# Kernel optimization log

Measured on AMD Instinct MI355X. Metric: run time of the kernel, lower is better.

Reference implementation:

```python
import jax, jax.numpy as jnp
import numpy as np

B, L, C = 8, 4096, 512
WS, SHIFT, H = 64, 32, 16
HD = C // H
HID = 4 * C


def _ln(x, w, b):
    m = x.mean(-1, keepdims=True)
    v = ((x - m) ** 2).mean(-1, keepdims=True)
    return (x - m) / jnp.sqrt(v + 1e-5) * w + b


def _attn_mask():
    # 0 / -100 mask for shifted windows, shape (nW, WS, WS)
    img = np.zeros((L,), np.float32)
    cnt = 0
    for s in (slice(0, L - WS), slice(L - WS, L - SHIFT), slice(L - SHIFT, L)):
        img[s] = cnt
        cnt += 1
    mw = img.reshape(L // WS, WS)
    d = mw[:, :, None] - mw[:, None, :]
    return jnp.asarray(np.where(d != 0, -100.0, 0.0).astype(np.float32))


def _cpb_coords():
    # log-spaced continuous relative coords, shape (2*WS-1, 1)
    r = np.arange(-(WS - 1), WS, dtype=np.float32) / (WS - 1) * 8.0
    t = np.sign(r) * np.log2(np.abs(r) + 1.0) / np.log2(8.0)
    return jnp.asarray(t[:, None].astype(np.float32))


def _rel_index():
    c = np.arange(WS)
    return jnp.asarray((c[:, None] - c[None, :] + WS - 1).astype(np.int32))


def setup_inputs():
    key = jax.random.key(0)
    ks = jax.random.split(key, 8)
    n = jax.random.normal
    return {
        "x": n(ks[0], (B, L, C), jnp.float32),
        "qkv_w": n(ks[1], (3 * C, C), jnp.float32) * 0.02,
        "q_bias": jnp.zeros((C,), jnp.float32),
        "v_bias": jnp.zeros((C,), jnp.float32),
        "logit_scale": jnp.log(10.0 * jnp.ones((H, 1, 1), jnp.float32)),
        "cpb_w1": n(ks[2], (512, 1), jnp.float32) * 0.02,
        "cpb_b1": jnp.zeros((512,), jnp.float32),
        "cpb_w2": n(ks[3], (H, 512), jnp.float32) * 0.02,
        "proj_w": n(ks[4], (C, C), jnp.float32) * 0.02,
        "proj_b": jnp.zeros((C,), jnp.float32),
        "norm1_w": jnp.ones((C,), jnp.float32),
        "norm1_b": jnp.zeros((C,), jnp.float32),
        "norm2_w": jnp.ones((C,), jnp.float32),
        "norm2_b": jnp.zeros((C,), jnp.float32),
        "fc1_w": n(ks[5], (HID, C), jnp.float32) * 0.02,
        "fc1_b": jnp.zeros((HID,), jnp.float32),
        "fc2_w": n(ks[6], (C, HID), jnp.float32) * 0.02,
        "fc2_b": jnp.zeros((C,), jnp.float32),
    }


def reference(x, qkv_w, q_bias, v_bias, logit_scale, cpb_w1, cpb_b1, cpb_w2,
              proj_w, proj_b, norm1_w, norm1_b, norm2_w, norm2_b,
              fc1_w, fc1_b, fc2_w, fc2_b):
    nW = L // WS
    shortcut = x
    # cyclic shift + window partition
    xs = jnp.roll(x, -SHIFT, axis=1)
    xw = xs.reshape(B * nW, WS, C)
    # qkv with q/v bias only (k bias is zero)
    qkv_b = jnp.concatenate([q_bias, jnp.zeros_like(v_bias), v_bias])
    qkv = (xw @ qkv_w.T + qkv_b).reshape(B * nW, WS, 3, H, HD)
    qkv = qkv.transpose(2, 0, 3, 1, 4)  # (3, B*nW, H, WS, HD)
    q, k, v = qkv[0], qkv[1], qkv[2]
    # cosine attention with learned, clamped per-head temperature
    qn = q / jnp.maximum(jnp.linalg.norm(q, axis=-1, keepdims=True), 1e-12)
    kn = k / jnp.maximum(jnp.linalg.norm(k, axis=-1, keepdims=True), 1e-12)
    attn = jnp.einsum('whnd,whmd->whnm', qn, kn)
    scale = jnp.exp(jnp.minimum(logit_scale, jnp.log(100.0)))  # (H,1,1)
    attn = attn * scale
    # continuous relative position bias via small MLP
    tbl = jax.nn.relu(_cpb_coords() @ cpb_w1.T + cpb_b1) @ cpb_w2.T  # (2WS-1, H)
    bias = tbl[_rel_index()]  # (WS, WS, H)
    bias = 16.0 * jax.nn.sigmoid(bias.transpose(2, 0, 1))  # (H, WS, WS)
    attn = attn + bias[None]
    # shift mask (0 / -100), per window
    mask = _attn_mask()  # (nW, WS, WS)
    attn = attn.reshape(B, nW, H, WS, WS) + mask[None, :, None]
    attn = jax.nn.softmax(attn.reshape(B * nW, H, WS, WS), axis=-1)
    out = jnp.einsum('whnm,whmd->whnd', attn, v)
    out = out.transpose(0, 2, 1, 3).reshape(B * nW, WS, C)
    out = out @ proj_w.T + proj_b
    # window reverse + reverse shift
    out = jnp.roll(out.reshape(B, L, C), SHIFT, axis=1)
    # Swin v2 post-norm residuals
    x1 = shortcut + _ln(out, norm1_w, norm1_b)
    h = jax.nn.gelu(x1 @ fc1_w.T + fc1_b, approximate=False) @ fc2_w.T + fc2_b
    return x1 + _ln(h, norm2_w, norm2_b)
```

## Files before the change

kernel.cpp:

```cpp
#include <hip/hip_runtime.h>
#include <hip/hip_bf16.h>
#include <math.h>

typedef unsigned short u16;
typedef __bf16 bf16x8 __attribute__((ext_vector_type(8)));
typedef float f32x4 __attribute__((ext_vector_type(4)));
typedef unsigned short u16x8 __attribute__((ext_vector_type(8)));
typedef unsigned short u16x4 __attribute__((ext_vector_type(4)));
typedef unsigned short u16x2 __attribute__((ext_vector_type(2)));

#define DEV static __device__ __forceinline__

DEV float b2f(u16 v) { unsigned u = ((unsigned)v) << 16; return __builtin_bit_cast(float, u); }
DEV u16 f2bf(float f) {
  unsigned u = __builtin_bit_cast(unsigned, f);
  u += 0x7fffu + ((u >> 16) & 1u);
  return (u16)(u >> 16);
}

DEV void async16(const void* g, void* l) {
  __builtin_amdgcn_global_load_lds(
      (const __attribute__((address_space(1))) void*)g,
      (__attribute__((address_space(3))) void*)l, 16, 0, 0);
}

__global__ __launch_bounds__(256) void cvt_kernel(
    const float* __restrict__ in, u16* __restrict__ out, int n4)
{
  const int i = blockIdx.x * 256 + threadIdx.x;
  if (i < n4) {
    float4 v = ((const float4*)in)[i];
    u16x4 o;
    o[0] = f2bf(v.x); o[1] = f2bf(v.y); o[2] = f2bf(v.z); o[3] = f2bf(v.w);
    ((u16x4*)out)[i] = o;
  }
}

__global__ __launch_bounds__(64) void cpb_kernel(
    const float* __restrict__ w1, const float* __restrict__ b1,
    const float* __restrict__ w2, float* __restrict__ btbl)
{
  const int h = blockIdx.x;
  const int lane = threadIdx.x;
  __shared__ float tbl[127];
  for (int r = lane; r < 127; r += 64) {
    float rv = (float)(r - 63) * (8.0f / 63.0f);
    float sgn = (rv > 0.f) ? 1.f : ((rv < 0.f) ? -1.f : 0.f);
    float t = sgn * log2f(fabsf(rv) + 1.f) * (1.f / 3.f);
    float acc = 0.f;
    for (int k = 0; k < 512; ++k) {
      float hid = fmaxf(t * w1[k] + b1[k], 0.f);
      acc += hid * w2[h * 512 + k];
    }
    tbl[r] = acc;
  }
  __syncthreads();
  for (int idx = lane; idx < 4096; idx += 64) {
    int i = idx >> 6, j = idx & 63;
    float v = tbl[i - j + 63];
    btbl[h * 4096 + idx] = 16.f / (1.f + __expf(-v));
  }
}

template <int MODE>
__global__ __launch_bounds__(512, 2) void gemm_bt(
    const u16* __restrict__ A, const u16* __restrict__ W,
    const float* __restrict__ bias1, const float* __restrict__ bias2,
    u16* __restrict__ out, int M, int N, int K)
{
  extern __shared__ __attribute__((aligned(16))) u16 smem[];
  const int tid = threadIdx.x;
  const int lane = tid & 63;
  const int wv = tid >> 6;
  const int m0 = blockIdx.x * 256;
  const int n0 = blockIdx.y * 256;
  const int wm = (wv >> 2) * 128;
  const int wn = (wv & 3) * 64;
  const int fr = lane & 15;
  const int hi = lane >> 4;
  const int srow = tid >> 3;
  const int kb = (tid & 7) ^ (srow & 7);
  f32x4 acc[8][4] = {};

  auto stageA = [&](int buf, int k0, int i) {
    const int r = srow + (i << 6);
    const u16* src;
    if constexpr (MODE == 0) {
      const int mg = m0 + r;
      const int bb = mg >> 12;
      const int p = mg & 4095;
      const long ga = ((long)bb << 12) + ((p + 32) & 4095);
      src = A + ga * (long)K + k0 + kb * 8;
    } else if constexpr (MODE == 1) {
      const int kk = k0 + kb * 8;
      src = A + (size_t)(kk >> 5) * 1048576 + (size_t)(m0 + r) * 32 + (kk & 31);
    } else {
      src = A + (size_t)(m0 + r) * K + k0 + kb * 8;
    }
    async16(src, smem + buf * 16384 + ((i << 9) + tid) * 8);
  };
  auto stageB = [&](int buf, int k0, int i) {
    const int r = srow + (i << 6);
    async16(W + (size_t)(n0 + r) * K + k0 + kb * 8,
            smem + 32768 + buf * 16384 + ((i << 9) + tid) * 8);
  };
  auto stage_part = [&](int buf, int k0, int part) {
    if (part == 0)      { stageB(buf, k0, 0); stageB(buf, k0, 1); }
    else if (part == 1) { stageB(buf, k0, 2); stageB(buf, k0, 3); }
    else if (part == 2) { stageA(buf, k0, 0); stageA(buf, k0, 2); }
    else                { stageA(buf, k0, 1); stageA(buf, k0, 3); }
  };

  auto phase_compute = [&](const u16* lac, const u16* lbc, int mh, int ks) {
    bf16x8 fa[4], fb[4];
    const int sw = hi + (ks << 2);
    #pragma unroll
    for (int mi = 0; mi < 4; ++mi) {
      const int r = wm + ((mh << 2) + mi) * 16 + fr;
      fa[mi] = *(const bf16x8*)&lac[r * 64 + ((sw ^ (r & 7)) << 3)];
    }
    #pragma unroll
    for (int ni = 0; ni < 4; ++ni) {
      const int r = wn + ni * 16 + fr;
      fb[ni] = *(const bf16x8*)&lbc[r * 64 + ((sw ^ (r & 7)) << 3)];
    }
    asm volatile("s_waitcnt lgkmcnt(0)" ::: "memory");
    __builtin_amdgcn_sched_barrier(0);
    __builtin_amdgcn_s_setprio(1);
    #pragma unroll
    for (int mi = 0; mi < 4; ++mi)
      #pragma unroll
      for (int ni = 0; ni < 4; ++ni)
        acc[(mh << 2) + mi][ni] = __builtin_amdgcn_mfma_f32_16x16x32_bf16(
            fa[mi], fb[ni], acc[(mh << 2) + mi][ni], 0, 0, 0);
    __builtin_amdgcn_s_setprio(0);
  };

  const int NT = K >> 6;
  stage_part(0, 0, 0); stage_part(0, 0, 1); stage_part(0, 0, 2); stage_part(0, 0, 3);
  int cur = 0;
  for (int kt = 0; kt < NT; ++kt) {
    const bool hn = (kt + 1) < NT;
    const int nk0 = (kt + 1) << 6;
    const u16* lac = smem + cur * 16384;
    const u16* lbc = smem + 32768 + cur * 16384;
    const int nb = cur ^ 1;
    asm volatile("s_waitcnt vmcnt(2)" ::: "memory");
    __builtin_amdgcn_s_barrier();
    if (hn) stage_part(nb, nk0, 0);
    phase_compute(lac, lbc, 0, 0);
    if (hn) { asm volatile("s_waitcnt vmcnt(2)" ::: "memory"); }
    else    { asm volatile("s_waitcnt vmcnt(0)" ::: "memory"); }
    __builtin_amdgcn_s_barrier();
    if (hn) stage_part(nb, nk0, 1);
    phase_compute(lac, lbc, 1, 0);
    if (hn) stage_part(nb, nk0, 2);
    phase_compute(lac, lbc, 0, 1);
    if (hn) stage_part(nb, nk0, 3);
    phase_compute(lac, lbc, 1, 1);
    cur ^= 1;
  }

  const int lrow = hi * 4;
  #pragma unroll
  for (int mi = 0; mi < 8; ++mi) {
    #pragma unroll
    for (int ni = 0; ni < 4; ++ni) {
      const int n = n0 + wn + ni * 16 + fr;
      #pragma unroll
      for (int r = 0; r < 4; ++r) {
        const int m = m0 + wm + mi * 16 + lrow + r;
        float v = acc[mi][ni][r];
        if constexpr (MODE == 0) {
          const int which = n >> 9, c = n & 511;
          const int hh = c >> 5, d = c & 31;
          float bias = (which == 0) ? bias1[c] : (which == 2 ? bias2[c] : 0.f);
          const int g = m >> 6, ii = m & 63;
          out[(size_t)which * 16777216 + (size_t)g * 32768 + hh * 2048 + ii * 32 + d] =
              f2bf(v + bias);
        } else if constexpr (MODE == 2) {
          float t = v + bias1[n];
          float u = t * t;
          float z = t * (1.5957691216f + 0.0713548163f * u);
          float ge = t / (1.f + __expf(-z));
          out[(size_t)m * N + n] = f2bf(ge);
        } else {
          out[(size_t)m * N + n] = f2bf(v + bias1[n]);
        }
      }
    }
  }
}

__global__ __launch_bounds__(256) void gemm_sm3(
    const u16* __restrict__ A, const u16* __restrict__ W,
    const float* __restrict__ bias1,
    u16* __restrict__ out, int M, int N, int K)
{
  __shared__ __attribute__((aligned(16))) u16 lA[2][8192];
  __shared__ __attribute__((aligned(16))) u16 lB[2][8192];
  const int tid = threadIdx.x;
  const int wid = tid >> 6;
  const int lane = tid & 63;
  const int m0 = blockIdx.x * 128;
  const int n0 = blockIdx.y * 128;
  const int wm = (wid >> 1) * 64;
  const int wn = (wid & 1) * 64;
  f32x4 acc[4][4] = {};

  const int srow8 = lane >> 3;
  const int kel = ((lane & 7) ^ srow8) * 8;

  auto stage = [&](int b, int k0) {
    #pragma unroll
    for (int cc = 0; cc < 4; ++cc) {
      const int rb = wid * 32 + cc * 8;
      const int r = rb + srow8;
      async16(A + (size_t)(m0 + r) * K + k0 + kel, &lA[b][rb * 64]);
      async16(W + (size_t)(n0 + r) * K + k0 + kel, &lB[b][rb * 64]);
    }
  };

  const int NT = K >> 6;
  stage(0, 0);
  __syncthreads();
  int cur = 0;
  const int fr = lane & 15;
  const int hi = lane >> 4;
  const int fsw = fr & 7;
  for (int kt = 0; kt < NT; ++kt) {
    if (kt + 1 < NT) stage(cur ^ 1, (kt + 1) << 6);
    #pragma unroll
    for (int ks = 0; ks < 2; ++ks) {
      bf16x8 fa[4], fb[4];
      #pragma unroll
      for (int t = 0; t < 4; ++t) {
        const int ra = wm + t * 16 + fr;
        fa[t] = *(const bf16x8*)&lA[cur][ra * 64 + (((hi + 4 * ks) ^ fsw) << 3)];
        const int rbq = wn + t * 16 + fr;
        fb[t] = *(const bf16x8*)&lB[cur][rbq * 64 + (((hi + 4 * ks) ^ fsw) << 3)];
      }
      #pragma unroll
      for (int mi = 0; mi < 4; ++mi)
        #pragma unroll
        for (int ni = 0; ni < 4; ++ni)
          acc[mi][ni] = __builtin_amdgcn_mfma_f32_16x16x32_bf16(fa[mi], fb[ni], acc[mi][ni], 0, 0, 0);
    }
    __syncthreads();
    cur ^= 1;
  }

  const int lrow = (lane >> 4) * 4;
  #pragma unroll
  for (int mi = 0; mi < 4; ++mi)
    #pragma unroll
    for (int ni = 0; ni < 4; ++ni) {
      const int n = n0 + wn + ni * 16 + fr;
      #pragma unroll
      for (int r = 0; r < 4; ++r) {
        const int m = m0 + wm + mi * 16 + lrow + r;
        out[(size_t)m * N + n] = f2bf(acc[mi][ni][r] + bias1[n]);
      }
    }
}

__global__ __launch_bounds__(256) void attn_kernel(
    const u16* __restrict__ qkv, const float* __restrict__ ls,
    const float* __restrict__ btbl, u16* __restrict__ attnT)
{
  const int gg = blockIdx.x;
  const int w = threadIdx.x >> 6;
  const int lane = threadIdx.x & 63;
  __shared__ __attribute__((aligned(16))) u16 vt[4][2048];
  __shared__ __attribute__((aligned(16))) u16 pl[4][4096];
  const bool maskw = ((gg & 63) == 63);
  const int fr = lane & 15;
  const int fkq = (lane >> 4) * 8;
  const int crow = (lane >> 4) * 4;

  for (int t = 0; t < 4; ++t) {
    const int h = w * 4 + t;
    const size_t bgh = (size_t)gg * 32768 + (size_t)h * 2048;

    {
      const u16x8* vp = (const u16x8*)(qkv + 33554432 + bgh + (size_t)lane * 32);
      #pragma unroll
      for (int c = 0; c < 4; ++c) {
        u16x8 vr = vp[c];
        #pragma unroll
        for (int e = 0; e < 8; ++e) {
          const int d = c * 8 + e;
          const int addr = d * 64 + (((lane >> 3) ^ (d & 7)) << 3) + (lane & 7);
          vt[w][addr] = vr[e];
        }
      }
    }

    const float scale = __expf(fminf(ls[h], 4.6051701859880914f));
    bf16x8 qa[4], kb[4];
    #pragma unroll
    for (int mi = 0; mi < 4; ++mi) {
      u16x8 raw = *(const u16x8*)(qkv + bgh + (size_t)(mi * 16 + fr) * 32 + fkq);
      float f[8]; float ssum = 0.f;
      #pragma unroll
      for (int e = 0; e < 8; ++e) { f[e] = b2f(raw[e]); ssum += f[e] * f[e]; }
      ssum += __shfl_xor(ssum, 16); ssum += __shfl_xor(ssum, 32);
      const float mul = scale / fmaxf(sqrtf(ssum), 1e-12f);
      u16x8 tmp;
      #pragma unroll
      for (int e = 0; e < 8; ++e) tmp[e] = f2bf(f[e] * mul);
      qa[mi] = __builtin_bit_cast(bf16x8, tmp);
    }
    #pragma unroll
    for (int ni = 0; ni < 4; ++ni) {
      u16x8 raw = *(const u16x8*)(qkv + 16777216 + bgh + (size_t)(ni * 16 + fr) * 32 + fkq);
      float f[8]; float ssum = 0.f;
      #pragma unroll
      for (int e = 0; e < 8; ++e) { f[e] = b2f(raw[e]); ssum += f[e] * f[e]; }
      ssum += __shfl_xor(ssum, 16); ssum += __shfl_xor(ssum, 32);
      const float mul = 1.f / fmaxf(sqrtf(ssum), 1e-12f);
      u16x8 tmp;
      #pragma unroll
      for (int e = 0; e < 8; ++e) tmp[e] = f2bf(f[e] * mul);
      kb[ni] = __builtin_bit_cast(bf16x8, tmp);
    }

    f32x4 s[4][4] = {};
    __builtin_amdgcn_s_setprio(1);
    #pragma unroll
    for (int mi = 0; mi < 4; ++mi)
      #pragma unroll
      for (int ni = 0; ni < 4; ++ni)
        s[mi][ni] = __builtin_amdgcn_mfma_f32_16x16x32_bf16(qa[mi], kb[ni], s[mi][ni], 0, 0, 0);
    __builtin_amdgcn_s_setprio(0);

    const float mh = scale + 16.f;
    float inv_[4][4];
    #pragma unroll
    for (int mi = 0; mi < 4; ++mi) {
      #pragma unroll
      for (int r = 0; r < 4; ++r) {
        const int row = mi * 16 + crow + r;
        float es = 0.f;
        #pragma unroll
        for (int ni = 0; ni < 4; ++ni) {
          const int col = ni * 16 + fr;
          float sv = s[mi][ni][r] + btbl[h * 4096 + row * 64 + col];
          if (maskw && ((row < 32) != (col < 32))) sv -= 100.f;
          const float e = __expf(sv - mh);
          s[mi][ni][r] = e;
          es += e;
        }
        es += __shfl_xor(es, 1); es += __shfl_xor(es, 2);
        es += __shfl_xor(es, 4); es += __shfl_xor(es, 8);
        inv_[mi][r] = 1.f / fmaxf(es, 1e-37f);
      }
    }

    #pragma unroll
    for (int mi = 0; mi < 4; ++mi)
      #pragma unroll
      for (int r = 0; r < 4; ++r) {
        const int row = mi * 16 + crow + r;
        #pragma unroll
        for (int ni = 0; ni < 4; ++ni) {
          const int col = ni * 16 + fr;
          const int addr = row * 64 + (((col >> 3) ^ (row & 7)) << 3) + (col & 7);
          pl[w][addr] = f2bf(s[mi][ni][r]);
        }
      }
    __syncthreads();

    f32x4 o[4][2] = {};
    #pragma unroll
    for (int ks = 0; ks < 2; ++ks) {
      bf16x8 vbf[2];
      #pragma unroll
      for (int np = 0; np < 2; ++np) {
        const int d = np * 16 + fr;
        const int jb = (lane >> 4) + ks * 4;
        vbf[np] = *(const bf16x8*)&vt[w][d * 64 + ((jb ^ (d & 7)) << 3)];
      }
      __builtin_amdgcn_s_setprio(1);
      #pragma unroll
      for (int mp = 0; mp < 4; ++mp) {
        const int row = mp * 16 + fr;
        const int cb = (lane >> 4) + ks * 4;
        bf16x8 paf = *(const bf16x8*)&pl[w][row * 64 + ((cb ^ (row & 7)) << 3)];
        o[mp][0] = __builtin_amdgcn_mfma_f32_16x16x32_bf16(paf, vbf[0], o[mp][0], 0, 0, 0);
        o[mp][1] = __builtin_amdgcn_mfma_f32_16x16x32_bf16(paf, vbf[1], o[mp][1], 0, 0, 0);
      }
      __builtin_amdgcn_s_setprio(0);
    }

    #pragma unroll
    for (int mp = 0; mp < 4; ++mp)
      #pragma unroll
      for (int r = 0; r < 4; ++r) {
        const int row = mp * 16 + crow + r;
        const float iv = inv_[mp][r];
        u16* op = attnT + (size_t)h * 1048576 + (size_t)(gg * 64 + row) * 32;
        op[fr]      = f2bf(o[mp][0][r] * iv);
        op[16 + fr] = f2bf(o[mp][1][r] * iv);
      }
    __syncthreads();
  }
}

__global__ __launch_bounds__(256) void ln1_kernel(
    const u16* __restrict__ proj, const float* __restrict__ x,
    const float* __restrict__ w, const float* __restrict__ bb,
    u16* __restrict__ x1h)
{
  const int t = blockIdx.x;
  const int b = t >> 12, l = t & 4095;
  const int p = (l - 32) & 4095;
  const size_t srow = (((size_t)b << 12) + p) << 9;
  const int c0 = threadIdx.x * 2;
  u16x2 pv = *(const u16x2*)(proj + srow + c0);
  float v0 = b2f(pv[0]), v1 = b2f(pv[1]);
  float s = v0 + v1, ss = v0 * v0 + v1 * v1;
  #pragma unroll
  for (int o = 32; o > 0; o >>= 1) { s += __shfl_down(s, o); ss += __shfl_down(ss, o); }
  __shared__ float red[8];
  const int wid = threadIdx.x >> 6, lane = threadIdx.x & 63;
  if (lane == 0) { red[wid] = s; red[4 + wid] = ss; }
  __syncthreads();
  const float S = red[0] + red[1] + red[2] + red[3];
  const float SS = red[4] + red[5] + red[6] + red[7];
  const float mean = S * (1.f / 512.f);
  const float var = SS * (1.f / 512.f) - mean * mean;
  const float rstd = rsqrtf(var + 1e-5f);
  const size_t orow = (size_t)t << 9;
  float2 xv = *(const float2*)(x + orow + c0);
  const float r0 = xv.x + (v0 - mean) * rstd * w[c0] + bb[c0];
  const float r1 = xv.y + (v1 - mean) * rstd * w[c0 + 1] + bb[c0 + 1];
  u16x2 ho; ho[0] = f2bf(r0); ho[1] = f2bf(r1);
  *(u16x2*)(x1h + orow + c0) = ho;
}

__global__ __launch_bounds__(256) void ln2_kernel(
    const u16* __restrict__ fc2, const u16* __restrict__ x1h,
    const float* __restrict__ w, const float* __restrict__ bb,
    float* __restrict__ out)
{
  const int t = blockIdx.x;
  const size_t row = (size_t)t << 9;
  const int c0 = threadIdx.x * 2;
  u16x2 pv = *(const u16x2*)(fc2 + row + c0);
  float v0 = b2f(pv[0]), v1 = b2f(pv[1]);
  float s = v0 + v1, ss = v0 * v0 + v1 * v1;
  #pragma unroll
  for (int o = 32; o > 0; o >>= 1) { s += __shfl_down(s, o); ss += __shfl_down(ss, o); }
  __shared__ float red[8];
  const int wid = threadIdx.x >> 6, lane = threadIdx.x & 63;
  if (lane == 0) { red[wid] = s; red[4 + wid] = ss; }
  __syncthreads();
  const float S = red[0] + red[1] + red[2] + red[3];
  const float SS = red[4] + red[5] + red[6] + red[7];
  const float mean = S * (1.f / 512.f);
  const float var = SS * (1.f / 512.f) - mean * mean;
  const float rstd = rsqrtf(var + 1e-5f);
  u16x2 xv = *(const u16x2*)(x1h + row + c0);
  const float r0 = b2f(xv[0]) + (v0 - mean) * rstd * w[c0] + bb[c0];
  const float r1 = b2f(xv[1]) + (v1 - mean) * rstd * w[c0 + 1] + bb[c0 + 1];
  float2 fo; fo.x = r0; fo.y = r1;
  *(float2*)(out + row + c0) = fo;
}

extern "C" void kernel_launch(void* const* d_in, const int* in_sizes, int n_in,
                              void* d_out, int out_size, void* d_ws, size_t ws_size,
                              hipStream_t stream) {
  const float* x        = (const float*)d_in[0];
  const float* qkv_w    = (const float*)d_in[1];
  const float* q_bias   = (const float*)d_in[2];
  const float* v_bias   = (const float*)d_in[3];
  const float* lscale   = (const float*)d_in[4];
  const float* cpb_w1   = (const float*)d_in[5];
  const float* cpb_b1   = (const float*)d_in[6];
  const float* cpb_w2   = (const float*)d_in[7];
  const float* proj_w   = (const float*)d_in[8];
  const float* proj_b   = (const float*)d_in[9];
  const float* n1w      = (const float*)d_in[10];
  const float* n1b      = (const float*)d_in[11];
  const float* n2w      = (const float*)d_in[12];
  const float* n2b      = (const float*)d_in[13];
  const float* fc1_w    = (const float*)d_in[14];
  const float* fc1_b    = (const float*)d_in[15];
  const float* fc2_w    = (const float*)d_in[16];
  const float* fc2_b    = (const float*)d_in[17];

  if (ws_size < 134217728u) return;
  char* ws = (char*)d_ws;
  u16* wqkv   = (u16*)(ws + 0);
  u16* wproj  = (u16*)(ws + 1572864);
  u16* wfc1   = (u16*)(ws + 2097152);
  u16* wfc2   = (u16*)(ws + 4194304);
  float* btbl = (float*)(ws + 6291456);
  u16* qkv    = (u16*)(ws + 6553600);
  u16* projo  = (u16*)(ws + 6553600);
  u16* hbuf   = (u16*)(ws + 6553600);
  u16* fc2oh  = (u16*)(ws + 73662464);
  u16* x1h    = (u16*)(ws + 94371840);
  u16* xbf   = (u16*)d_out;
  u16* attnT = (u16*)d_out;
  float* out = (float*)d_out;

  hipFuncSetAttribute((const void*)gemm_bt<0>, hipFuncAttributeMaxDynamicSharedMemorySize, 131072);
  hipFuncSetAttribute((const void*)gemm_bt<1>, hipFuncAttributeMaxDynamicSharedMemorySize, 131072);
  hipFuncSetAttribute((const void*)gemm_bt<2>, hipFuncAttributeMaxDynamicSharedMemorySize, 131072);

  cpb_kernel<<<16, 64, 0, stream>>>(cpb_w1, cpb_b1, cpb_w2, btbl);
  cvt_kernel<<<768, 256, 0, stream>>>(qkv_w, wqkv, 196608);
  cvt_kernel<<<256, 256, 0, stream>>>(proj_w, wproj, 65536);
  cvt_kernel<<<1024, 256, 0, stream>>>(fc1_w, wfc1, 262144);
  cvt_kernel<<<1024, 256, 0, stream>>>(fc2_w, wfc2, 262144);
  cvt_kernel<<<16384, 256, 0, stream>>>(x, xbf, 4194304);

  gemm_bt<0><<<dim3(128, 6), 512, 131072, stream>>>(
      xbf, wqkv, q_bias, v_bias, qkv, 32768, 1536, 512);
  attn_kernel<<<512, 256, 0, stream>>>(qkv, lscale, btbl, attnT);
  gemm_bt<1><<<dim3(128, 2), 512, 131072, stream>>>(
      attnT, wproj, proj_b, nullptr, projo, 32768, 512, 512);
  ln1_kernel<<<32768, 256, 0, stream>>>(projo, x, n1w, n1b, x1h);
  for (int half = 0; half < 2; ++half) {
    const u16* a2 = x1h + (size_t)half * 8388608;
    gemm_bt<2><<<dim3(64, 8), 512, 131072, stream>>>(
        a2, wfc1, fc1_b, nullptr, hbuf, 16384, 2048, 512);
    gemm_sm3<<<dim3(128, 4), 256, 0, stream>>>(
        hbuf, wfc2, fc2_b, fc2oh, 16384, 512, 2048);
    ln2_kernel<<<16384, 256, 0, stream>>>(
        fc2oh, a2, n2w, n2b, out + (size_t)half * 8388608);
  }
}
```

Before: 464.4 us.

## Restructure gemm_bt LDS layout into k-halves, reuse B fragments, remap block order

The GEMM now stores each 64-wide K tile as two 32-column halves with a 4-slot swizzle. B fragments are loaded once per k-half and reused across both M halves instead of being reloaded every phase. Blocks are launched on a 1D grid whose index is permuted in groups of 8 (aimed at XCD/L2 locality), and the M/N tile is derived from that index. The pipeline gains extra barriers and different vmcnt waits, which adds sync overhead in exchange for fewer LDS reads and possibly better cache reuse.

```diff
diff --git a/kernel.cpp b/kernel.cpp
--- a/kernel.cpp
+++ b/kernel.cpp
@@ -62,67 +62,76 @@
   }
 }
 
+DEV int swzr(int r) { return (r + (r >> 2)) & 3; }
+
 template <int MODE>
 __global__ __launch_bounds__(512, 2) void gemm_bt(
     const u16* __restrict__ A, const u16* __restrict__ W,
     const float* __restrict__ bias1, const float* __restrict__ bias2,
-    u16* __restrict__ out, int M, int N, int K)
+    u16* __restrict__ out, int nby, int N, int K)
 {
   extern __shared__ __attribute__((aligned(16))) u16 smem[];
   const int tid = threadIdx.x;
   const int lane = tid & 63;
   const int wv = tid >> 6;
-  const int m0 = blockIdx.x * 256;
-  const int n0 = blockIdx.y * 256;
+  const int q8 = (int)gridDim.x >> 3;
+  const int swb = (blockIdx.x & 7) * q8 + (blockIdx.x >> 3);
+  const int m0 = (swb / nby) * 256;
+  const int n0 = (swb % nby) * 256;
   const int wm = (wv >> 2) * 128;
   const int wn = (wv & 3) * 64;
   const int fr = lane & 15;
   const int hi = lane >> 4;
-  const int srow = tid >> 3;
-  const int kb = (tid & 7) ^ (srow & 7);
+  const int sr = tid >> 2;
+  const int slot = tid & 3;
   f32x4 acc[8][4] = {};
-
-  auto stageA = [&](int buf, int k0, int i) {
-    const int r = srow + (i << 6);
+  bf16x8 fb[4];
+
+  auto stA = [&](int buf, int k0, int kh, int i) {
+    const int lr = i * 128 + sr;
+    const int kk = k0 + kh * 32 + ((slot ^ swzr(lr)) << 3);
     const u16* src;
     if constexpr (MODE == 0) {
-      const int mg = m0 + r;
+      const int mg = m0 + lr;
       const int bb = mg >> 12;
       const int p = mg & 4095;
       const long ga = ((long)bb << 12) + ((p + 32) & 4095);
-      src = A + ga * (long)K + k0 + kb * 8;
+      src = A + ga * (long)K + kk;
     } else if constexpr (MODE == 1) {
-      const int kk = k0 + kb * 8;
-      src = A + (size_t)(kk >> 5) * 1048576 + (size_t)(m0 + r) * 32 + (kk & 31);
+      src = A + (size_t)(kk >> 5) * 1048576 + (size_t)(m0 + lr) * 32 + (kk & 31);
     } else {
-      src = A + (size_t)(m0 + r) * K + k0 + kb * 8;
-    }
-    async16(src, smem + buf * 16384 + ((i << 9) + tid) * 8);
+      src = A + (size_t)(m0 + lr) * K + kk;
+    }
+    async16(src, smem + buf * 32768 + kh * 8192 + lr * 32 + slot * 8);
   };
-  auto stageB = [&](int buf, int k0, int i) {
-    const int r = srow + (i << 6);
-    async16(W + (size_t)(n0 + r) * K + k0 + kb * 8,
-            smem + 32768 + buf * 16384 + ((i << 9) + tid) * 8);
+  auto stB = [&](int buf, int k0, int kh, int i) {
+    const int lr = i * 128 + sr;
+    const int kk = k0 + kh * 32 + ((slot ^ swzr(lr)) << 3);
+    async16(W + (size_t)(n0 + lr) * K + kk,
+            smem + buf * 32768 + 16384 + kh * 8192 + lr * 32 + slot * 8);
   };
-  auto stage_part = [&](int buf, int k0, int part) {
-    if (part == 0)      { stageB(buf, k0, 0); stageB(buf, k0, 1); }
-    else if (part == 1) { stageB(buf, k0, 2); stageB(buf, k0, 3); }
-    else if (part == 2) { stageA(buf, k0, 0); stageA(buf, k0, 2); }
-    else                { stageA(buf, k0, 1); stageA(buf, k0, 3); }
+  auto stage_part = [&](int buf, int k0, int p) {
+    if (p == 0)      { stB(buf, k0, 0, 0); stB(buf, k0, 0, 1); }
+    else if (p == 1) { stA(buf, k0, 0, 0); stA(buf, k0, 0, 1); }
+    else if (p == 2) { stB(buf, k0, 1, 0); stB(buf, k0, 1, 1); }
+    else             { stA(buf, k0, 1, 0); stA(buf, k0, 1, 1); }
   };
 
-  auto phase_compute = [&](const u16* lac, const u16* lbc, int mh, int ks) {
-    bf16x8 fa[4], fb[4];
-    const int sw = hi + (ks << 2);
+  auto phase = [&](int buf, int mh, int ks, bool readB) {
+    const u16* baseA = smem + buf * 32768 + ks * 8192;
+    const u16* baseB = smem + buf * 32768 + 16384 + ks * 8192;
+    bf16x8 fa[4];
     #pragma unroll
     for (int mi = 0; mi < 4; ++mi) {
-      const int r = wm + ((mh << 2) + mi) * 16 + fr;
-      fa[mi] = *(const bf16x8*)&lac[r * 64 + ((sw ^ (r & 7)) << 3)];
-    }
-    #pragma unroll
-    for (int ni = 0; ni < 4; ++ni) {
-      const int r = wn + ni * 16 + fr;
-      fb[ni] = *(const bf16x8*)&lbc[r * 64 + ((sw ^ (r & 7)) << 3)];
+      const int lr = wm + mh * 64 + mi * 16 + fr;
+      fa[mi] = *(const bf16x8*)&baseA[lr * 32 + ((hi ^ swzr(lr)) << 3)];
+    }
+    if (readB) {
+      #pragma unroll
+      for (int ni = 0; ni < 4; ++ni) {
+        const int lr = wn + ni * 16 + fr;
+        fb[ni] = *(const bf16x8*)&baseB[lr * 32 + ((hi ^ swzr(lr)) << 3)];
+      }
     }
     asm volatile("s_waitcnt lgkmcnt(0)" ::: "memory");
     __builtin_amdgcn_sched_barrier(0);
@@ -138,27 +147,32 @@
 
   const int NT = K >> 6;
   stage_part(0, 0, 0); stage_part(0, 0, 1); stage_part(0, 0, 2); stage_part(0, 0, 3);
-  int cur = 0;
+
   for (int kt = 0; kt < NT; ++kt) {
+    const int cur = kt & 1;
+    const int nb = cur ^ 1;
     const bool hn = (kt + 1) < NT;
     const int nk0 = (kt + 1) << 6;
-    const u16* lac = smem + cur * 16384;
-    const u16* lbc = smem + 32768 + cur * 16384;
-    const int nb = cur ^ 1;
-    asm volatile("s_waitcnt vmcnt(2)" ::: "memory");
-    __builtin_amdgcn_s_barrier();
-    if (hn) stage_part(nb, nk0, 0);
-    phase_compute(lac, lbc, 0, 0);
-    if (hn) { asm volatile("s_waitcnt vmcnt(2)" ::: "memory"); }
+    if (hn) { stage_part(nb, nk0, 0);
+              asm volatile("s_waitcnt vmcnt(6)" ::: "memory"); }
+    else    { asm volatile("s_waitcnt vmcnt(4)" ::: "memory"); }
+    __builtin_amdgcn_s_barrier();
+    phase(cur, 0, 0, true);
+    __builtin_amdgcn_s_barrier();
+    if (hn) stage_part(nb, nk0, 1);
+    __builtin_amdgcn_s_barrier();
+    phase(cur, 1, 0, false);
+    __builtin_amdgcn_s_barrier();
+    if (hn) { stage_part(nb, nk0, 2);
+              asm volatile("s_waitcnt vmcnt(6)" ::: "memory"); }
     else    { asm volatile("s_waitcnt vmcnt(0)" ::: "memory"); }
     __builtin_amdgcn_s_barrier();
-    if (hn) stage_part(nb, nk0, 1);
-    phase_compute(lac, lbc, 1, 0);
-    if (hn) stage_part(nb, nk0, 2);
-    phase_compute(lac, lbc, 0, 1);
+    phase(cur, 0, 1, true);
+    __builtin_amdgcn_s_barrier();
     if (hn) stage_part(nb, nk0, 3);
-    phase_compute(lac, lbc, 1, 1);
-    cur ^= 1;
+    __builtin_amdgcn_s_barrier();
+    phase(cur, 1, 1, false);
+    __builtin_amdgcn_s_barrier();
   }
 
   const int lrow = hi * 4;
@@ -517,16 +531,16 @@
   cvt_kernel<<<1024, 256, 0, stream>>>(fc2_w, wfc2, 262144);
   cvt_kernel<<<16384, 256, 0, stream>>>(x, xbf, 4194304);
 
-  gemm_bt<0><<<dim3(128, 6), 512, 131072, stream>>>(
-      xbf, wqkv, q_bias, v_bias, qkv, 32768, 1536, 512);
+  gemm_bt<0><<<768, 512, 131072, stream>>>(
+      xbf, wqkv, q_bias, v_bias, qkv, 6, 1536, 512);
   attn_kernel<<<512, 256, 0, stream>>>(qkv, lscale, btbl, attnT);
-  gemm_bt<1><<<dim3(128, 2), 512, 131072, stream>>>(
-      attnT, wproj, proj_b, nullptr, projo, 32768, 512, 512);
+  gemm_bt<1><<<256, 512, 131072, stream>>>(
+      attnT, wproj, proj_b, nullptr, projo, 2, 512, 512);
   ln1_kernel<<<32768, 256, 0, stream>>>(projo, x, n1w, n1b, x1h);
   for (int half = 0; half < 2; ++half) {
     const u16* a2 = x1h + (size_t)half * 8388608;
-    gemm_bt<2><<<dim3(64, 8), 512, 131072, stream>>>(
-        a2, wfc1, fc1_b, nullptr, hbuf, 16384, 2048, 512);
+    gemm_bt<2><<<512, 512, 131072, stream>>>(
+        a2, wfc1, fc1_b, nullptr, hbuf, 8, 2048, 512);
     gemm_sm3<<<dim3(128, 4), 256, 0, stream>>>(
         hbuf, wfc2, fc2_b, fc2oh, 16384, 512, 2048);
     ln2_kernel<<<16384, 256, 0, stream>>>(
```

Result: slower. 488.1 us (+5.1%).

## Swizzle GEMM tile order for XCD locality and fuse conversion launches

Applied to the files above, without the earlier changes.

The GEMM kernels now use a 1D grid and remap block IDs so that consecutive blocks landing on the same XCD (blockIdx mod 8) cover neighbouring tiles that share A rows and W columns. This is meant to improve L2 reuse on the multi-die GPU. The five fp32-to-bf16 conversion launches are merged into one kernel. The relative-position-bias MLP is split into a parallel per-(r,h) reduction kernel plus an expansion kernel, replacing a serial 16-block kernel. The swizzle assumes the grid size is divisible by 8 and adds integer division per block.

```diff
diff --git a/kernel.cpp b/kernel.cpp
--- a/kernel.cpp
+++ b/kernel.cpp
@@ -24,40 +24,53 @@
       (__attribute__((address_space(3))) void*)l, 16, 0, 0);
 }
 
-__global__ __launch_bounds__(256) void cvt_kernel(
-    const float* __restrict__ in, u16* __restrict__ out, int n4)
+__global__ __launch_bounds__(256) void cvt_all_kernel(
+    const float* __restrict__ x,  const float* __restrict__ wq,
+    const float* __restrict__ wp, const float* __restrict__ w1,
+    const float* __restrict__ w2,
+    u16* __restrict__ dx, u16* __restrict__ dq, u16* __restrict__ dp,
+    u16* __restrict__ d1, u16* __restrict__ d2)
 {
   const int i = blockIdx.x * 256 + threadIdx.x;
-  if (i < n4) {
-    float4 v = ((const float4*)in)[i];
-    u16x4 o;
-    o[0] = f2bf(v.x); o[1] = f2bf(v.y); o[2] = f2bf(v.z); o[3] = f2bf(v.w);
-    ((u16x4*)out)[i] = o;
-  }
-}
-
-__global__ __launch_bounds__(64) void cpb_kernel(
+  const float* s; u16* d; int off;
+  if (i < 4194304)      { s = x;  d = dx; off = i; }
+  else if (i < 4390912) { s = wq; d = dq; off = i - 4194304; }
+  else if (i < 4456448) { s = wp; d = dp; off = i - 4390912; }
+  else if (i < 4718592) { s = w1; d = d1; off = i - 4456448; }
+  else if (i < 4980736) { s = w2; d = d2; off = i - 4718592; }
+  else return;
+  float4 v = ((const float4*)s)[off];
+  u16x4 o;
+  o[0] = f2bf(v.x); o[1] = f2bf(v.y); o[2] = f2bf(v.z); o[3] = f2bf(v.w);
+  ((u16x4*)d)[off] = o;
+}
+
+__global__ __launch_bounds__(64) void cpb1_kernel(
     const float* __restrict__ w1, const float* __restrict__ b1,
-    const float* __restrict__ w2, float* __restrict__ btbl)
+    const float* __restrict__ w2, float* __restrict__ tbl)
+{
+  const int r = blockIdx.x, h = blockIdx.y;
+  const int lane = threadIdx.x;
+  float rv = (float)(r - 63) * (8.0f / 63.0f);
+  float sgn = (rv > 0.f) ? 1.f : ((rv < 0.f) ? -1.f : 0.f);
+  float t = sgn * log2f(fabsf(rv) + 1.f) * (1.f / 3.f);
+  float part = 0.f;
+  for (int k = lane; k < 512; k += 64) {
+    float hid = fmaxf(t * w1[k] + b1[k], 0.f);
+    part += hid * w2[h * 512 + k];
+  }
+  #pragma unroll
+  for (int o = 32; o > 0; o >>= 1) part += __shfl_down(part, o);
+  if (lane == 0) tbl[r * 16 + h] = part;
+}
+
+__global__ __launch_bounds__(256) void cpb2_kernel(
+    const float* __restrict__ tbl, float* __restrict__ btbl)
 {
   const int h = blockIdx.x;
-  const int lane = threadIdx.x;
-  __shared__ float tbl[127];
-  for (int r = lane; r < 127; r += 64) {
-    float rv = (float)(r - 63) * (8.0f / 63.0f);
-    float sgn = (rv > 0.f) ? 1.f : ((rv < 0.f) ? -1.f : 0.f);
-    float t = sgn * log2f(fabsf(rv) + 1.f) * (1.f / 3.f);
-    float acc = 0.f;
-    for (int k = 0; k < 512; ++k) {
-      float hid = fmaxf(t * w1[k] + b1[k], 0.f);
-      acc += hid * w2[h * 512 + k];
-    }
-    tbl[r] = acc;
-  }
-  __syncthreads();
-  for (int idx = lane; idx < 4096; idx += 64) {
+  for (int idx = threadIdx.x; idx < 4096; idx += 256) {
     int i = idx >> 6, j = idx & 63;
-    float v = tbl[i - j + 63];
+    float v = tbl[(i - j + 63) * 16 + h];
     btbl[h * 4096 + idx] = 16.f / (1.f + __expf(-v));
   }
 }
@@ -66,14 +79,16 @@
 __global__ __launch_bounds__(512, 2) void gemm_bt(
     const u16* __restrict__ A, const u16* __restrict__ W,
     const float* __restrict__ bias1, const float* __restrict__ bias2,
-    u16* __restrict__ out, int M, int N, int K)
+    u16* __restrict__ out, int nby, int N, int K)
 {
   extern __shared__ __attribute__((aligned(16))) u16 smem[];
   const int tid = threadIdx.x;
   const int lane = tid & 63;
   const int wv = tid >> 6;
-  const int m0 = blockIdx.x * 256;
-  const int n0 = blockIdx.y * 256;
+  const int q8 = (int)gridDim.x >> 3;
+  const int swb = (blockIdx.x & 7) * q8 + (blockIdx.x >> 3);
+  const int m0 = (swb / nby) * 256;
+  const int n0 = (swb % nby) * 256;
   const int wm = (wv >> 2) * 128;
   const int wn = (wv & 3) * 64;
   const int fr = lane & 15;
@@ -195,15 +210,17 @@
 __global__ __launch_bounds__(256) void gemm_sm3(
     const u16* __restrict__ A, const u16* __restrict__ W,
     const float* __restrict__ bias1,
-    u16* __restrict__ out, int M, int N, int K)
+    u16* __restrict__ out, int nby, int N, int K)
 {
   __shared__ __attribute__((aligned(16))) u16 lA[2][8192];
   __shared__ __attribute__((aligned(16))) u16 lB[2][8192];
   const int tid = threadIdx.x;
   const int wid = tid >> 6;
   const int lane = tid & 63;
-  const int m0 = blockIdx.x * 128;
-  const int n0 = blockIdx.y * 128;
+  const int q8 = (int)gridDim.x >> 3;
+  const int swb = (blockIdx.x & 7) * q8 + (blockIdx.x >> 3);
+  const int m0 = (swb / nby) * 128;
+  const int n0 = (swb % nby) * 128;
   const int wm = (wid >> 1) * 64;
   const int wn = (wid & 1) * 64;
   f32x4 acc[4][4] = {};
@@ -502,6 +519,7 @@
   u16* hbuf   = (u16*)(ws + 6553600);
   u16* fc2oh  = (u16*)(ws + 73662464);
   u16* x1h    = (u16*)(ws + 94371840);
+  float* tbl  = (float*)(ws + 127926272);
   u16* xbf   = (u16*)d_out;
   u16* attnT = (u16*)d_out;
   float* out = (float*)d_out;
@@ -510,25 +528,23 @@
   hipFuncSetAttribute((const void*)gemm_bt<1>, hipFuncAttributeMaxDynamicSharedMemorySize, 131072);
   hipFuncSetAttribute((const void*)gemm_bt<2>, hipFuncAttributeMaxDynamicSharedMemorySize, 131072);
 
-  cpb_kernel<<<16, 64, 0, stream>>>(cpb_w1, cpb_b1, cpb_w2, btbl);
-  cvt_kernel<<<768, 256, 0, stream>>>(qkv_w, wqkv, 196608);
-  cvt_kernel<<<256, 256, 0, stream>>>(proj_w, wproj, 65536);
-  cvt_kernel<<<1024, 256, 0, stream>>>(fc1_w, wfc1, 262144);
-  cvt_kernel<<<1024, 256, 0, stream>>>(fc2_w, wfc2, 262144);
-  cvt_kernel<<<16384, 256, 0, stream>>>(x, xbf, 4194304);
-
-  gemm_bt<0><<<dim3(128, 6), 512, 131072, stream>>>(
-      xbf, wqkv, q_bias, v_bias, qkv, 32768, 1536, 512);
+  cvt_all_kernel<<<19456, 256, 0, stream>>>(
+      x, qkv_w, proj_w, fc1_w, fc2_w, xbf, wqkv, wproj, wfc1, wfc2);
+  cpb1_kernel<<<dim3(127, 16), 64, 0, stream>>>(cpb_w1, cpb_b1, cpb_w2, tbl);
+  cpb2_kernel<<<16, 256, 0, stream>>>(tbl, btbl);
+
+  gemm_bt<0><<<768, 512, 131072, stream>>>(
+      xbf, wqkv, q_bias, v_bias, qkv, 6, 1536, 512);
   attn_kernel<<<512, 256, 0, stream>>>(qkv, lscale, btbl, attnT);
-  gemm_bt<1><<<dim3(128, 2), 512, 131072, stream>>>(
-      attnT, wproj, proj_b, nullptr, projo, 32768, 512, 512);
+  gemm_bt<1><<<256, 512, 131072, stream>>>(
+      attnT, wproj, proj_b, nullptr, projo, 2, 512, 512);
   ln1_kernel<<<32768, 256, 0, stream>>>(projo, x, n1w, n1b, x1h);
   for (int half = 0; half < 2; ++half) {
     const u16* a2 = x1h + (size_t)half * 8388608;
-    gemm_bt<2><<<dim3(64, 8), 512, 131072, stream>>>(
-        a2, wfc1, fc1_b, nullptr, hbuf, 16384, 2048, 512);
-    gemm_sm3<<<dim3(128, 4), 256, 0, stream>>>(
-        hbuf, wfc2, fc2_b, fc2oh, 16384, 512, 2048);
+    gemm_bt<2><<<512, 512, 131072, stream>>>(
+        a2, wfc1, fc1_b, nullptr, hbuf, 8, 2048, 512);
+    gemm_sm3<<<512, 256, 0, stream>>>(
+        hbuf, wfc2, fc2_b, fc2oh, 4, 512, 2048);
     ln2_kernel<<<16384, 256, 0, stream>>>(
         fc2oh, a2, n2w, n2b, out + (size_t)half * 8388608);
   }
```

Measured after the change: 442.2 us. -4.8%, faster.
